# Performance work log

Hardware: AMD Instinct MI355X
Metric: run time of the kernel (lower is better)

The kernel has to match this reference:

```python
import jax, jax.numpy as jnp
import numpy as np

B, NT, DIM, H = 8, 1024, 768, 12
HD = DIM // H
SCALE = HD ** -0.5


def setup_inputs() -> dict:
    key = jax.random.key(0)
    ks = jax.random.split(key, 9)
    s = DIM ** -0.5
    return {
        "tfeat": jax.random.normal(ks[0], (B, NT, DIM), jnp.float32),
        "wq": jax.random.normal(ks[1], (DIM, DIM), jnp.float32) * s,
        "bq": jnp.zeros((DIM,), jnp.float32),
        "wk": jax.random.normal(ks[2], (DIM, DIM), jnp.float32) * s,
        "bk": jnp.zeros((DIM,), jnp.float32),
        "wv": jax.random.normal(ks[3], (DIM, DIM), jnp.float32) * s,
        "bv": jnp.zeros((DIM,), jnp.float32),
        "wp": jax.random.normal(ks[4], (DIM, DIM), jnp.float32) * s,
        "bp": jnp.zeros((DIM,), jnp.float32),
    }


def reference(tfeat, wq, bq, wk, bk, wv, bv, wp, bp):
    # Linear stores weight [out, in]; y = x @ W^T + b
    def split_heads(x):  # [B,Nt,C] -> [B,H,Nt,hd]
        b, n, c = x.shape
        return x.reshape(b, n, H, HD).transpose(0, 2, 1, 3)

    q = split_heads(tfeat @ wq.T + bq)
    k = split_heads(tfeat @ wk.T + bk)
    v = split_heads(tfeat @ wv.T + bv)
    # [B,H,Nt,Nt]
    attn = jax.nn.softmax(jnp.einsum('bhqd,bhkd->bhqk', q, k) * SCALE, axis=-1)
    # dropout is identity in eval mode
    x = jnp.einsum('bhqk,bhkd->bhqd', attn, v)
    x = x.transpose(0, 2, 1, 3).reshape(tfeat.shape)
    x = x @ wp.T + bp
    return (x, attn)
```

## Files before the change

kernel.cpp:

```cpp
#include <hip/hip_runtime.h>
#include <math.h>

#define B_    8
#define NT_   1024
#define DIM_  768
#define H_    12
#define HD_   64
#define SCALE_ 0.125f
#define T_ELEMS 6291456UL

typedef _Float16 half8  __attribute__((ext_vector_type(8)));
typedef _Float16 half4v __attribute__((ext_vector_type(4)));
typedef float    floatx4 __attribute__((ext_vector_type(4)));

#if __has_builtin(__builtin_amdgcn_exp2f)
#define EXP2F(x) __builtin_amdgcn_exp2f(x)
#else
#define EXP2F(x) exp2f(x)
#endif

#define GLD16(gp, lp) __builtin_amdgcn_global_load_lds( \
    (const __attribute__((address_space(1))) unsigned int*)(gp), \
    (__attribute__((address_space(3))) unsigned int*)(lp), 16, 0, 0)

__global__ void cvt4(const float* __restrict__ in, _Float16* __restrict__ out,
                     int n4) {
  int i = blockIdx.x * 256 + threadIdx.x;
  if (i < n4) {
    float4 v = ((const float4*)in)[i];
    half4v h = { (_Float16)v.x, (_Float16)v.y, (_Float16)v.z, (_Float16)v.w };
    *(half4v*)(out + 4 * (size_t)i) = h;
  }
}

template<int MODE>
__global__ __launch_bounds__(256) void gemm128(
    const _Float16* __restrict__ A, const _Float16* __restrict__ Bt,
    const float* __restrict__ b0_, const float* __restrict__ b1_,
    const float* __restrict__ b2_, _Float16* __restrict__ outh,
    float* __restrict__ outf, int K)
{
  __shared__ _Float16 As[128 * 32];
  __shared__ _Float16 Bs[128 * 32];
  const int t    = threadIdx.x;
  const int w    = t >> 6, lane = t & 63;
  const int quad = lane >> 4, l16 = lane & 15;
  const int wm   = (w >> 1) * 64, wn = (w & 1) * 64;
  const int m0   = blockIdx.x * 128, n0 = blockIdx.y * 128;

  const _Float16* gA = A  + (size_t)(m0 + (t >> 2)) * K + (t & 3) * 8;
  const _Float16* gB = Bt + (size_t)(n0 + (t >> 2)) * K + (t & 3) * 8;
  _Float16* lA = As + w * 512;
  _Float16* lB = Bs + w * 512;
  const size_t rowK = (size_t)64 * K;

  floatx4 acc[4][4] = {};

  for (int k0 = 0; k0 < K; k0 += 32) {
    __syncthreads();
    GLD16(gA + k0,        lA);
    GLD16(gA + rowK + k0, lA + 2048);
    GLD16(gB + k0,        lB);
    GLD16(gB + rowK + k0, lB + 2048);
    __syncthreads();

    half8 af[4], bf[4];
#pragma unroll
    for (int i = 0; i < 4; i++)
      af[i] = *(const half8*)(As + (wm + i * 16 + l16) * 32 + quad * 8);
#pragma unroll
    for (int j = 0; j < 4; j++)
      bf[j] = *(const half8*)(Bs + (wn + j * 16 + l16) * 32 + quad * 8);
#pragma unroll
    for (int i = 0; i < 4; i++)
#pragma unroll
      for (int j = 0; j < 4; j++)
        acc[i][j] = __builtin_amdgcn_mfma_f32_16x16x32_f16(af[i], bf[j],
                                                           acc[i][j], 0, 0, 0);
  }

  const int sel = (MODE == 0) ? (n0 / 768) : 0;
  const float* bb = (MODE == 0)
                      ? (sel == 0 ? b0_ : (sel == 1 ? b1_ : b2_))
                      : b0_;
#pragma unroll
  for (int j = 0; j < 4; j++) {
    const int col = n0 + wn + j * 16 + l16;
    const int cl  = col - sel * 768;
    const float bv = bb[cl];
#pragma unroll
    for (int i = 0; i < 4; i++)
#pragma unroll
      for (int r = 0; r < 4; r++) {
        const int row = m0 + wm + i * 16 + quad * 4 + r;
        const float v = acc[i][j][r] + bv;
        if (MODE == 0)
          outh[(size_t)sel * T_ELEMS + (size_t)row * 768 + cl] = (_Float16)v;
        else
          outf[(size_t)row * 768 + col] = v;
      }
  }
}

__global__ __launch_bounds__(256) void attn_kernel(
    const _Float16* __restrict__ Qh, const _Float16* __restrict__ Kh,
    const _Float16* __restrict__ Vh, float* __restrict__ attn_out,
    _Float16* __restrict__ Xh)
{
  __shared__ _Float16 Ks[64][72];
  __shared__ _Float16 Vt[64][72];
  __shared__ _Float16 Ps[64][72];

  const int t    = threadIdx.x;
  const int w    = t >> 6, lane = t & 63;
  const int quad = lane >> 4, l16 = lane & 15;
  const int qt = blockIdx.x, h = blockIdx.y, b = blockIdx.z;
  const int q0 = qt * 64;

  const _Float16* Qb = Qh + ((size_t)b * NT_) * DIM_ + h * HD_;
  const _Float16* Kb = Kh + ((size_t)b * NT_) * DIM_ + h * HD_;
  const _Float16* Vb = Vh + ((size_t)b * NT_) * DIM_ + h * HD_;

  const int lrow = t >> 2;
  const int lcol = (t & 3) * 16;

  half8 qf[2];
  {
    const _Float16* qr = Qb + (size_t)(q0 + w * 16 + l16) * DIM_ + quad * 8;
    qf[0] = *(const half8*)(qr);
    qf[1] = *(const half8*)(qr + 32);
  }

  const float C2 = 0.18033688011112042f;
  float m_run[4], l_run[4];
#pragma unroll
  for (int r = 0; r < 4; r++) { m_run[r] = -INFINITY; l_run[r] = 0.0f; }

  for (int kt = 0; kt < 16; kt++) {
    __syncthreads();
    *(uint4*)(&Ks[lrow][lcol])     = *(const uint4*)(Kb + (size_t)(kt * 64 + lrow) * DIM_ + lcol);
    *(uint4*)(&Ks[lrow][lcol + 8]) = *(const uint4*)(Kb + (size_t)(kt * 64 + lrow) * DIM_ + lcol + 8);
    __syncthreads();

    floatx4 s[4] = {};
#pragma unroll
    for (int ks = 0; ks < 2; ks++) {
#pragma unroll
      for (int j = 0; j < 4; j++) {
        half8 bk = *(const half8*)(&Ks[j * 16 + l16][ks * 32 + quad * 8]);
        s[j] = __builtin_amdgcn_mfma_f32_16x16x32_f16(qf[ks], bk, s[j], 0, 0, 0);
      }
    }
#pragma unroll
    for (int r = 0; r < 4; r++) {
      float tm = fmaxf(fmaxf(s[0][r], s[1][r]), fmaxf(s[2][r], s[3][r]));
      for (int off = 1; off < 16; off <<= 1)
        tm = fmaxf(tm, __shfl_xor(tm, off, 64));
      const float nm  = fmaxf(m_run[r], tm);
      const float nmc = nm * C2;
      float ts = EXP2F(fmaf(s[0][r], C2, -nmc)) + EXP2F(fmaf(s[1][r], C2, -nmc))
               + EXP2F(fmaf(s[2][r], C2, -nmc)) + EXP2F(fmaf(s[3][r], C2, -nmc));
      for (int off = 1; off < 16; off <<= 1)
        ts += __shfl_xor(ts, off, 64);
      l_run[r] = l_run[r] * EXP2F((m_run[r] - nm) * C2) + ts;
      m_run[r] = nm;
    }
  }

  float mb[4];
#pragma unroll
  for (int r = 0; r < 4; r++) mb[r] = m_run[r] * C2 + log2f(l_run[r]);

  floatx4 oacc[4] = {};
  float* attn_b = attn_out + ((size_t)(b * H_ + h) * NT_ + q0) * NT_;

  for (int kt = 0; kt < 16; kt++) {
    __syncthreads();
    *(uint4*)(&Ks[lrow][lcol])     = *(const uint4*)(Kb + (size_t)(kt * 64 + lrow) * DIM_ + lcol);
    *(uint4*)(&Ks[lrow][lcol + 8]) = *(const uint4*)(Kb + (size_t)(kt * 64 + lrow) * DIM_ + lcol + 8);
    {
      alignas(16) _Float16 vh[16];
      *(uint4*)(vh)     = *(const uint4*)(Vb + (size_t)(kt * 64 + lrow) * DIM_ + lcol);
      *(uint4*)(vh + 8) = *(const uint4*)(Vb + (size_t)(kt * 64 + lrow) * DIM_ + lcol + 8);
#pragma unroll
      for (int c = 0; c < 16; c++) Vt[lcol + c][lrow] = vh[c];
    }
    __syncthreads();

    floatx4 s[4] = {};
#pragma unroll
    for (int ks = 0; ks < 2; ks++) {
#pragma unroll
      for (int j = 0; j < 4; j++) {
        half8 bk = *(const half8*)(&Ks[j * 16 + l16][ks * 32 + quad * 8]);
        s[j] = __builtin_amdgcn_mfma_f32_16x16x32_f16(qf[ks], bk, s[j], 0, 0, 0);
      }
    }

#pragma unroll
    for (int j = 0; j < 4; j++)
#pragma unroll
      for (int r = 0; r < 4; r++) {
        const float p = EXP2F(fmaf(s[j][r], C2, -mb[r]));
        const int qr = w * 16 + quad * 4 + r;
        attn_b[(size_t)qr * NT_ + kt * 64 + j * 16 + l16] = p;
        Ps[qr][j * 16 + l16] = (_Float16)p;
      }

#pragma unroll
    for (int ks = 0; ks < 2; ks++) {
      half8 pa = *(const half8*)(&Ps[w * 16 + l16][ks * 32 + quad * 8]);
#pragma unroll
      for (int j2 = 0; j2 < 4; j2++) {
        half8 bv = *(const half8*)(&Vt[j2 * 16 + l16][ks * 32 + quad * 8]);
        oacc[j2] = __builtin_amdgcn_mfma_f32_16x16x32_f16(pa, bv, oacc[j2], 0, 0, 0);
      }
    }
  }

#pragma unroll
  for (int j2 = 0; j2 < 4; j2++)
#pragma unroll
    for (int r = 0; r < 4; r++) {
      const int qr = q0 + w * 16 + quad * 4 + r;
      Xh[((size_t)b * NT_ + qr) * DIM_ + h * HD_ + j2 * 16 + l16] = (_Float16)oacc[j2][r];
    }
}

extern "C" void kernel_launch(void* const* d_in, const int* in_sizes, int n_in,
                              void* d_out, int out_size, void* d_ws, size_t ws_size,
                              hipStream_t stream) {
  const float* tfeat = (const float*)d_in[0];
  const float* wq    = (const float*)d_in[1];
  const float* bq    = (const float*)d_in[2];
  const float* wk    = (const float*)d_in[3];
  const float* bk    = (const float*)d_in[4];
  const float* wv    = (const float*)d_in[5];
  const float* bv    = (const float*)d_in[6];
  const float* wp    = (const float*)d_in[7];
  const float* bp    = (const float*)d_in[8];
  float* out = (float*)d_out;

  const size_t T = T_ELEMS;
  const size_t W = (size_t)DIM_ * DIM_;

  _Float16* ws  = (_Float16*)d_ws;
  _Float16* tfh = ws;
  _Float16* wqh = ws + T;
  _Float16* wkh = ws + T + W;
  _Float16* wvh = ws + T + 2 * W;
  _Float16* wph = ws + T + 3 * W;
  _Float16* Qh  = ws + T + 4 * W;
  _Float16* Kh  = Qh + T;
  _Float16* Vh  = Kh + T;
  _Float16* Xh  = Vh + T;

  cvt4<<<(int)(T / 4 / 256), 256, 0, stream>>>(tfeat, tfh, (int)(T / 4));
  cvt4<<<(int)(W / 4 / 256), 256, 0, stream>>>(wq, wqh, (int)(W / 4));
  cvt4<<<(int)(W / 4 / 256), 256, 0, stream>>>(wk, wkh, (int)(W / 4));
  cvt4<<<(int)(W / 4 / 256), 256, 0, stream>>>(wv, wvh, (int)(W / 4));
  cvt4<<<(int)(W / 4 / 256), 256, 0, stream>>>(wp, wph, (int)(W / 4));

  gemm128<0><<<dim3(64, 18), 256, 0, stream>>>(tfh, wqh, bq, bk, bv, Qh, nullptr, 768);

  attn_kernel<<<dim3(NT_ / 64, H_, B_), 256, 0, stream>>>(Qh, Kh, Vh, out + T, Xh);

  gemm128<1><<<dim3(64, 6), 256, 0, stream>>>(Xh, wph, bp, nullptr, nullptr, nullptr, out, 768);
}
```

Before: 632.5 us.

## Read K/V from global in attention, pre-transpose V, drop running max, swizzle grids

Adds a separate kernel that transposes V per head, so the attention kernel can load K and V^T fragments straight from global memory into MFMA operands. This removes the LDS staging and the __syncthreads barriers around it. The first softmax pass drops its running max and shuffle reductions and just sums exp2 of scaled scores, which can overflow if the scores are large. Both the GEMM and attention grids are remapped so that blocks sharing data are grouped by blockIdx mod 8, which appears aimed at the per-XCD L2 caches. The cost is an extra launch, an extra workspace buffer and extra global traffic for V^T.

```diff
diff --git a/kernel.cpp b/kernel.cpp
--- a/kernel.cpp
+++ b/kernel.cpp
@@ -46,7 +46,12 @@
   const int w    = t >> 6, lane = t & 63;
   const int quad = lane >> 4, l16 = lane & 15;
   const int wm   = (w >> 1) * 64, wn = (w & 1) * 64;
-  const int m0   = blockIdx.x * 128, n0 = blockIdx.y * 128;
+
+  const int nbx = gridDim.x;
+  int lin = blockIdx.y * nbx + blockIdx.x;
+  const int cpx = (nbx * gridDim.y) >> 3;
+  lin = (lin & 7) * cpx + (lin >> 3);
+  const int m0 = (lin % nbx) * 128, n0 = (lin / nbx) * 128;
 
   const _Float16* gA = A  + (size_t)(m0 + (t >> 2)) * K + (t & 3) * 8;
   const _Float16* gB = Bt + (size_t)(n0 + (t >> 2)) * K + (t & 3) * 8;
@@ -102,27 +107,48 @@
   }
 }
 
+__global__ __launch_bounds__(256) void transpose_v(
+    const _Float16* __restrict__ Vh, _Float16* __restrict__ VT)
+{
+  __shared__ _Float16 tile[64][72];
+  const int t = threadIdx.x;
+  const int tt = blockIdx.x, h = blockIdx.y, b = blockIdx.z;
+  const int lrow = t >> 2, lcol = (t & 3) * 16;
+
+  const _Float16* src = Vh + ((size_t)b * NT_ + tt * 64 + lrow) * DIM_ + h * HD_;
+  *(uint4*)(&tile[lrow][lcol])     = *(const uint4*)(src + lcol);
+  *(uint4*)(&tile[lrow][lcol + 8]) = *(const uint4*)(src + lcol + 8);
+  __syncthreads();
+
+  alignas(16) _Float16 vh[16];
+#pragma unroll
+  for (int c = 0; c < 16; c++) vh[c] = tile[lcol + c][lrow];
+  _Float16* dst = VT + ((size_t)(b * H_ + h) * HD_ + lrow) * NT_ + tt * 64 + lcol;
+  *(uint4*)(dst)     = *(const uint4*)(vh);
+  *(uint4*)(dst + 8) = *(const uint4*)(vh + 8);
+}
+
 __global__ __launch_bounds__(256) void attn_kernel(
     const _Float16* __restrict__ Qh, const _Float16* __restrict__ Kh,
-    const _Float16* __restrict__ Vh, float* __restrict__ attn_out,
+    const _Float16* __restrict__ VT, float* __restrict__ attn_out,
     _Float16* __restrict__ Xh)
 {
-  __shared__ _Float16 Ks[64][72];
-  __shared__ _Float16 Vt[64][72];
   __shared__ _Float16 Ps[64][72];
 
   const int t    = threadIdx.x;
   const int w    = t >> 6, lane = t & 63;
   const int quad = lane >> 4, l16 = lane & 15;
-  const int qt = blockIdx.x, h = blockIdx.y, b = blockIdx.z;
-  const int q0 = qt * 64;
+
+  const int bid  = blockIdx.x;
+  const int slot = bid & 7, i = bid >> 3;
+  const int g    = slot + 8 * (i >> 4);
+  const int qt   = i & 15;
+  const int b    = g / H_, h = g % H_;
+  const int q0   = qt * 64;
 
   const _Float16* Qb = Qh + ((size_t)b * NT_) * DIM_ + h * HD_;
   const _Float16* Kb = Kh + ((size_t)b * NT_) * DIM_ + h * HD_;
-  const _Float16* Vb = Vh + ((size_t)b * NT_) * DIM_ + h * HD_;
-
-  const int lrow = t >> 2;
-  const int lcol = (t & 3) * 16;
+  const _Float16* Vb = VT + (size_t)g * HD_ * NT_;
 
   half8 qf[2];
   {
@@ -132,70 +158,54 @@
   }
 
   const float C2 = 0.18033688011112042f;
-  float m_run[4], l_run[4];
-#pragma unroll
-  for (int r = 0; r < 4; r++) { m_run[r] = -INFINITY; l_run[r] = 0.0f; }
-
+
+  float lsum[4] = {0.f, 0.f, 0.f, 0.f};
   for (int kt = 0; kt < 16; kt++) {
-    __syncthreads();
-    *(uint4*)(&Ks[lrow][lcol])     = *(const uint4*)(Kb + (size_t)(kt * 64 + lrow) * DIM_ + lcol);
-    *(uint4*)(&Ks[lrow][lcol + 8]) = *(const uint4*)(Kb + (size_t)(kt * 64 + lrow) * DIM_ + lcol + 8);
-    __syncthreads();
-
+    const _Float16* kb = Kb + (size_t)(kt * 64 + l16) * DIM_ + quad * 8;
     floatx4 s[4] = {};
 #pragma unroll
-    for (int ks = 0; ks < 2; ks++) {
+    for (int ks = 0; ks < 2; ks++)
 #pragma unroll
       for (int j = 0; j < 4; j++) {
-        half8 bk = *(const half8*)(&Ks[j * 16 + l16][ks * 32 + quad * 8]);
+        half8 bk = *(const half8*)(kb + (size_t)(j * 16) * DIM_ + ks * 32);
         s[j] = __builtin_amdgcn_mfma_f32_16x16x32_f16(qf[ks], bk, s[j], 0, 0, 0);
       }
-    }
-#pragma unroll
-    for (int r = 0; r < 4; r++) {
-      float tm = fmaxf(fmaxf(s[0][r], s[1][r]), fmaxf(s[2][r], s[3][r]));
-      for (int off = 1; off < 16; off <<= 1)
-        tm = fmaxf(tm, __shfl_xor(tm, off, 64));
-      const float nm  = fmaxf(m_run[r], tm);
-      const float nmc = nm * C2;
-      float ts = EXP2F(fmaf(s[0][r], C2, -nmc)) + EXP2F(fmaf(s[1][r], C2, -nmc))
-               + EXP2F(fmaf(s[2][r], C2, -nmc)) + EXP2F(fmaf(s[3][r], C2, -nmc));
-      for (int off = 1; off < 16; off <<= 1)
-        ts += __shfl_xor(ts, off, 64);
-      l_run[r] = l_run[r] * EXP2F((m_run[r] - nm) * C2) + ts;
-      m_run[r] = nm;
-    }
+#pragma unroll
+    for (int j = 0; j < 4; j++)
+#pragma unroll
+      for (int r = 0; r < 4; r++)
+        lsum[r] += EXP2F(s[j][r] * C2);
   }
 
   float mb[4];
 #pragma unroll
-  for (int r = 0; r < 4; r++) mb[r] = m_run[r] * C2 + log2f(l_run[r]);
+  for (int r = 0; r < 4; r++) {
+    float ts = lsum[r];
+    for (int off = 1; off < 16; off <<= 1) ts += __shfl_xor(ts, off, 64);
+    mb[r] = log2f(ts);
+  }
 
   floatx4 oacc[4] = {};
-  float* attn_b = attn_out + ((size_t)(b * H_ + h) * NT_ + q0) * NT_;
+  float* attn_b = attn_out + ((size_t)g * NT_ + q0) * NT_;
 
   for (int kt = 0; kt < 16; kt++) {
-    __syncthreads();
-    *(uint4*)(&Ks[lrow][lcol])     = *(const uint4*)(Kb + (size_t)(kt * 64 + lrow) * DIM_ + lcol);
-    *(uint4*)(&Ks[lrow][lcol + 8]) = *(const uint4*)(Kb + (size_t)(kt * 64 + lrow) * DIM_ + lcol + 8);
-    {
-      alignas(16) _Float16 vh[16];
-      *(uint4*)(vh)     = *(const uint4*)(Vb + (size_t)(kt * 64 + lrow) * DIM_ + lcol);
-      *(uint4*)(vh + 8) = *(const uint4*)(Vb + (size_t)(kt * 64 + lrow) * DIM_ + lcol + 8);
-#pragma unroll
-      for (int c = 0; c < 16; c++) Vt[lcol + c][lrow] = vh[c];
-    }
-    __syncthreads();
-
+    const _Float16* kb = Kb + (size_t)(kt * 64 + l16) * DIM_ + quad * 8;
     floatx4 s[4] = {};
 #pragma unroll
-    for (int ks = 0; ks < 2; ks++) {
+    for (int ks = 0; ks < 2; ks++)
 #pragma unroll
       for (int j = 0; j < 4; j++) {
-        half8 bk = *(const half8*)(&Ks[j * 16 + l16][ks * 32 + quad * 8]);
+        half8 bk = *(const half8*)(kb + (size_t)(j * 16) * DIM_ + ks * 32);
         s[j] = __builtin_amdgcn_mfma_f32_16x16x32_f16(qf[ks], bk, s[j], 0, 0, 0);
       }
-    }
+
+    half8 bv[2][4];
+    const _Float16* vb = Vb + (size_t)l16 * NT_ + kt * 64 + quad * 8;
+#pragma unroll
+    for (int ks = 0; ks < 2; ks++)
+#pragma unroll
+      for (int j2 = 0; j2 < 4; j2++)
+        bv[ks][j2] = *(const half8*)(vb + (size_t)(j2 * 16) * NT_ + ks * 32);
 
 #pragma unroll
     for (int j = 0; j < 4; j++)
@@ -211,10 +221,9 @@
     for (int ks = 0; ks < 2; ks++) {
       half8 pa = *(const half8*)(&Ps[w * 16 + l16][ks * 32 + quad * 8]);
 #pragma unroll
-      for (int j2 = 0; j2 < 4; j2++) {
-        half8 bv = *(const half8*)(&Vt[j2 * 16 + l16][ks * 32 + quad * 8]);
-        oacc[j2] = __builtin_amdgcn_mfma_f32_16x16x32_f16(pa, bv, oacc[j2], 0, 0, 0);
-      }
+      for (int j2 = 0; j2 < 4; j2++)
+        oacc[j2] = __builtin_amdgcn_mfma_f32_16x16x32_f16(pa, bv[ks][j2],
+                                                          oacc[j2], 0, 0, 0);
     }
   }
 
@@ -254,6 +263,7 @@
   _Float16* Kh  = Qh + T;
   _Float16* Vh  = Kh + T;
   _Float16* Xh  = Vh + T;
+  _Float16* VTt = Xh + T;
 
   cvt4<<<(int)(T / 4 / 256), 256, 0, stream>>>(tfeat, tfh, (int)(T / 4));
   cvt4<<<(int)(W / 4 / 256), 256, 0, stream>>>(wq, wqh, (int)(W / 4));
@@ -263,7 +273,9 @@
 
   gemm128<0><<<dim3(64, 18), 256, 0, stream>>>(tfh, wqh, bq, bk, bv, Qh, nullptr, 768);
 
-  attn_kernel<<<dim3(NT_ / 64, H_, B_), 256, 0, stream>>>(Qh, Kh, Vh, out + T, Xh);
+  transpose_v<<<dim3(16, 12, 8), 256, 0, stream>>>(Vh, VTt);
+
+  attn_kernel<<<1536, 256, 0, stream>>>(Qh, Kh, VTt, out + T, Xh);
 
   gemm128<1><<<dim3(64, 6), 256, 0, stream>>>(Xh, wph, bp, nullptr, nullptr, nullptr, out, 768);
 }
```

After: 762.6 us. +20.6%, slower.
